# Kernel tuning notes

Measured on AMD Instinct MI355X. Metric: run time of the kernel, lower is better.

The kernel has to match this reference:

```python
import jax, jax.numpy as jnp
import numpy as np

N_NODES = 50000
N_EDGES = 600000
VOCAB = 32000
D = 128


def setup_inputs() -> dict:
    key = jax.random.key(0)
    ks = jax.random.split(key, 9)
    return {
        "emb_table": jax.random.normal(ks[0], (VOCAB, D), dtype=jnp.float32),
        "w1": jax.random.normal(ks[1], (D, D), dtype=jnp.float32) * (1.0 / np.sqrt(D)),
        "bias1": jax.random.normal(ks[2], (D,), dtype=jnp.float32),
        "w2": jax.random.normal(ks[3], (D, D), dtype=jnp.float32) * (1.0 / np.sqrt(D)),
        "bias2": jax.random.normal(ks[4], (D,), dtype=jnp.float32),
        "node_tokens": jax.random.randint(ks[5], (N_NODES,), 0, VOCAB, dtype=jnp.int32),
        "edge_tokens": jax.random.randint(ks[6], (N_EDGES,), 0, VOCAB, dtype=jnp.int32),
        "src": jax.random.randint(ks[7], (N_EDGES,), 0, N_NODES, dtype=jnp.int32),
        "dst": jax.random.randint(ks[8], (N_EDGES,), 0, N_NODES, dtype=jnp.int32),
    }


def reference(emb_table, w1, bias1, w2, bias2, node_tokens, edge_tokens, src, dst):
    # Embedding lookup + affine + relu for nodes and edges
    node_h = jax.nn.relu(emb_table[node_tokens] @ w1 + bias1)   # [N, D]
    edge_h = jax.nn.relu(emb_table[edge_tokens] @ w2 + bias2)   # [E, D]
    # DGL update_all(u_mul_e, sum): gather src node h, mul with edge h, scatter-sum to dst
    msg = node_h[src] * edge_h                                  # [E, D]
    out = jax.ops.segment_sum(msg, dst, num_segments=N_NODES)   # [N, D]
    return out
```

## Files before the change

### kernel.cpp

```cpp
#include <hip/hip_runtime.h>

#define VOCAB   32000
#define D       128
#define NNODES  50000
#define NEDGES  600000

typedef unsigned short ushort_t;
typedef unsigned int   uint_t;

__device__ __forceinline__ float bf2f(ushort_t u) {
    union { uint_t i; float f; } c; c.i = ((uint_t)u) << 16; return c.f;
}
__device__ __forceinline__ ushort_t f2bf(float f) {
    union { float f; uint_t i; } c; c.f = f;
    uint_t u = c.i;
    u += 0x7fff + ((u >> 16) & 1);
    return (ushort_t)(u >> 16);
}

__global__ __launch_bounds__(256) void mlp_hist_kernel(
    const float* __restrict__ emb,
    const float* __restrict__ w1, const float* __restrict__ b1,
    const float* __restrict__ w2, const float* __restrict__ b2,
    ushort_t* __restrict__ t1, ushort_t* __restrict__ t2,
    const int* __restrict__ dstv, int* __restrict__ counts)
{
    {
        const int base = blockIdx.x * (NEDGES / 1000);
        for (int i = base + threadIdx.x; i < base + NEDGES / 1000; i += 256)
            atomicAdd(&counts[dstv[i]], 1);
    }

    const int tab = (blockIdx.x >= 500) ? 1 : 0;
    const float* __restrict__ w = tab ? w2 : w1;
    const float* __restrict__ b = tab ? b2 : b1;
    ushort_t* __restrict__ outt = tab ? t2 : t1;
    const int bid = blockIdx.x - tab * 500;

    __shared__ __align__(16) float wT[D * D];

    {
        const int k0 = threadIdx.x >> 5;
        const int c4 = (threadIdx.x & 31) * 4;
        for (int kk = 0; kk < D; kk += 8) {
            const int k = kk + k0;
            const float4 v = *(const float4*)(w + (size_t)k * D + c4);
            const float vv[4] = {v.x, v.y, v.z, v.w};
            #pragma unroll
            for (int j = 0; j < 4; ++j) {
                const int c = c4 + j;
                const int g = (k >> 2) ^ (c & 7);
                wT[c * D + g * 4 + (k & 3)] = vv[j];
            }
        }
    }

    const int lane = threadIdx.x & 63;
    const int sub  = threadIdx.x >> 6;
    const int c0 = lane, c1 = lane + 64;
    const float bb0 = b[c0], bb1 = b[c1];
    const int s0 = (c0 & 7), s1 = (c1 & 7);
    __syncthreads();

    for (int it = 0; it < 4; ++it) {
        const int rowbase = __builtin_amdgcn_readfirstlane(
            (it * 500 + bid) * 16 + sub * 4);
        const float* __restrict__ x0 = emb + (size_t)rowbase * D;

        float acc[4][2];
        #pragma unroll
        for (int j = 0; j < 4; ++j) { acc[j][0] = bb0; acc[j][1] = bb1; }

        #pragma unroll 2
        for (int kc = 0; kc < 16; ++kc) {
            const int g0 = kc * 2, g1 = kc * 2 + 1;
            const float4 w0a = *(const float4*)&wT[c0 * D + ((g0 ^ s0) << 2)];
            const float4 w0b = *(const float4*)&wT[c0 * D + ((g1 ^ s0) << 2)];
            const float4 w1a = *(const float4*)&wT[c1 * D + ((g0 ^ s1) << 2)];
            const float4 w1b = *(const float4*)&wT[c1 * D + ((g1 ^ s1) << 2)];
            #pragma unroll
            for (int j = 0; j < 4; ++j) {
                const float* __restrict__ xr = x0 + j * D + kc * 8;
                const float4 xa = *(const float4*)(xr);
                const float4 xb = *(const float4*)(xr + 4);
                acc[j][0] = fmaf(xa.x, w0a.x, acc[j][0]);
                acc[j][1] = fmaf(xa.x, w1a.x, acc[j][1]);
                acc[j][0] = fmaf(xa.y, w0a.y, acc[j][0]);
                acc[j][1] = fmaf(xa.y, w1a.y, acc[j][1]);
                acc[j][0] = fmaf(xa.z, w0a.z, acc[j][0]);
                acc[j][1] = fmaf(xa.z, w1a.z, acc[j][1]);
                acc[j][0] = fmaf(xa.w, w0a.w, acc[j][0]);
                acc[j][1] = fmaf(xa.w, w1a.w, acc[j][1]);
                acc[j][0] = fmaf(xb.x, w0b.x, acc[j][0]);
                acc[j][1] = fmaf(xb.x, w1b.x, acc[j][1]);
                acc[j][0] = fmaf(xb.y, w0b.y, acc[j][0]);
                acc[j][1] = fmaf(xb.y, w1b.y, acc[j][1]);
                acc[j][0] = fmaf(xb.z, w0b.z, acc[j][0]);
                acc[j][1] = fmaf(xb.z, w1b.z, acc[j][1]);
                acc[j][0] = fmaf(xb.w, w0b.w, acc[j][0]);
                acc[j][1] = fmaf(xb.w, w1b.w, acc[j][1]);
            }
        }
        #pragma unroll
        for (int j = 0; j < 4; ++j) {
            ushort_t* o = outt + (size_t)(rowbase + j) * D;
            o[c0] = f2bf(fmaxf(acc[j][0], 0.f));
            o[c1] = f2bf(fmaxf(acc[j][1], 0.f));
        }
    }
}

__global__ __launch_bounds__(256) void scan_phase1(
    const int* __restrict__ counts,
    int* __restrict__ offs,
    int* __restrict__ btot)
{
    const int i    = blockIdx.x * 256 + threadIdx.x;
    const int lane = threadIdx.x & 63;
    const int wv   = threadIdx.x >> 6;

    const int v = (i < NNODES) ? counts[i] : 0;
    int inc = v;
    #pragma unroll
    for (int off = 1; off < 64; off <<= 1) {
        int u = __shfl_up(inc, off);
        if (lane >= off) inc += u;
    }
    __shared__ int wtot[4];
    if (lane == 63) wtot[wv] = inc;
    __syncthreads();
    int wpre = 0;
    #pragma unroll
    for (int k = 0; k < 3; ++k) if (k < wv) wpre += wtot[k];
    inc += wpre;
    if (i < NNODES) offs[i] = inc - v;
    if (threadIdx.x == 255) btot[blockIdx.x] = inc;
}

__global__ __launch_bounds__(256) void scan_phase2(
    const int* __restrict__ btot,
    int* __restrict__ offs,
    int* __restrict__ cursor,
    int nblocks)
{
    const int t    = threadIdx.x;
    const int lane = t & 63;
    const int wv   = t >> 6;

    int v = (t < blockIdx.x && t < nblocks) ? btot[t] : 0;
    #pragma unroll
    for (int off = 32; off > 0; off >>= 1) v += __shfl_xor(v, off);
    __shared__ int ws[4];
    if (lane == 0) ws[wv] = v;
    __syncthreads();
    const int bpre = ws[0] + ws[1] + ws[2] + ws[3];

    const int i = blockIdx.x * 256 + t;
    if (i < NNODES) {
        const int o = offs[i] + bpre;
        offs[i]   = o;
        cursor[i] = o;
    }
    if (blockIdx.x == 0 && t == 0) offs[NNODES] = NEDGES;
}

__global__ __launch_bounds__(256) void scatter_kernel(
    const int4* __restrict__ src4, const int4* __restrict__ dst4,
    const int* __restrict__ node_tokens, const int4* __restrict__ et4,
    int* __restrict__ cursor, uint_t* __restrict__ pairs)
{
    const int t = blockIdx.x * 256 + threadIdx.x;
    if (t >= NEDGES / 4) return;
    const int4 s = src4[t];
    const int4 d = dst4[t];
    const int4 te = et4[t];
    int p;
    p = atomicAdd(&cursor[d.x], 1);
    pairs[p] = (uint_t)node_tokens[s.x] | ((uint_t)te.x << 16);
    p = atomicAdd(&cursor[d.y], 1);
    pairs[p] = (uint_t)node_tokens[s.y] | ((uint_t)te.y << 16);
    p = atomicAdd(&cursor[d.z], 1);
    pairs[p] = (uint_t)node_tokens[s.z] | ((uint_t)te.z << 16);
    p = atomicAdd(&cursor[d.w], 1);
    pairs[p] = (uint_t)node_tokens[s.w] | ((uint_t)te.w << 16);
}

__global__ __launch_bounds__(256) void gather_kernel(
    const ushort_t* __restrict__ t1, const ushort_t* __restrict__ t2,
    const int* __restrict__ offsets, const uint_t* __restrict__ pairs,
    float* __restrict__ outp)
{
    const int wid = (blockIdx.x * 256 + threadIdx.x) >> 6;
    if (wid >= NNODES) return;
    const int lane = threadIdx.x & 63;
    const int half = lane >> 5;
    const int sl   = lane & 31;

    const int beg = offsets[wid];
    const int end = offsets[wid + 1];

    float4 acc = {0.f, 0.f, 0.f, 0.f};
    for (int base = beg; base < end; base += 64) {
        const int m = min(64, end - base);
        uint_t pr = (lane < m) ? pairs[base + lane] : 0u;
        for (int j = half; j < m; j += 2) {
            const uint_t v = (uint_t)__shfl((int)pr, j);
            const int tn = (int)(v & 0xffffu);
            const int te = (int)(v >> 16);
            const ushort4 a  = ((const ushort4*)(t1 + (size_t)tn * D))[sl];
            const ushort4 bb = ((const ushort4*)(t2 + (size_t)te * D))[sl];
            acc.x = fmaf(bf2f(a.x), bf2f(bb.x), acc.x);
            acc.y = fmaf(bf2f(a.y), bf2f(bb.y), acc.y);
            acc.z = fmaf(bf2f(a.z), bf2f(bb.z), acc.z);
            acc.w = fmaf(bf2f(a.w), bf2f(bb.w), acc.w);
        }
    }
    acc.x += __shfl_xor(acc.x, 32);
    acc.y += __shfl_xor(acc.y, 32);
    acc.z += __shfl_xor(acc.z, 32);
    acc.w += __shfl_xor(acc.w, 32);
    if (half == 0)
        ((float4*)(outp + (size_t)wid * D))[sl] = acc;
}

extern "C" void kernel_launch(void* const* d_in, const int* in_sizes, int n_in,
                              void* d_out, int out_size, void* d_ws, size_t ws_size,
                              hipStream_t stream) {
    const float* emb = (const float*)d_in[0];
    const float* w1  = (const float*)d_in[1];
    const float* b1  = (const float*)d_in[2];
    const float* w2  = (const float*)d_in[3];
    const float* b2  = (const float*)d_in[4];
    const int* node_tokens = (const int*)d_in[5];
    const int* edge_tokens = (const int*)d_in[6];
    const int* src = (const int*)d_in[7];
    const int* dst = (const int*)d_in[8];
    float* out = (float*)d_out;

    char* wsb = (char*)d_ws;
    ushort_t* t1     = (ushort_t*)(wsb);
    ushort_t* t2     = (ushort_t*)(wsb +  8192000);
    uint_t*   pairs  = (uint_t*)  (wsb + 16384000);
    int*      counts = (int*)     (wsb + 18784000);
    int*      offs   = (int*)     (wsb + 18984000);
    int*      cursor = (int*)     (wsb + 19184016);
    int*      btot   = (int*)     (wsb + 19384016);

    hipMemsetAsync(counts, 0, NNODES * sizeof(int), stream);

    mlp_hist_kernel<<<1000, 256, 0, stream>>>(emb, w1, b1, w2, b2,
                                              t1, t2, dst, counts);

    const int nscan = (NNODES + 255) / 256;
    scan_phase1<<<nscan, 256, 0, stream>>>(counts, offs, btot);
    scan_phase2<<<nscan, 256, 0, stream>>>(btot, offs, cursor, nscan);
    scatter_kernel<<<(NEDGES / 4 + 255) / 256, 256, 0, stream>>>(
        (const int4*)src, (const int4*)dst, node_tokens,
        (const int4*)edge_tokens, cursor, pairs);

    gather_kernel<<<(NNODES + 3) / 4, 256, 0, stream>>>(t1, t2, offs, pairs, out);
}
```

Baseline: 242.8 us.

## Compute vocab-table MLP with bf16 MFMA instead of scalar FMA

Replaces the scalar-FMA dense layer that precomputes relu(emb@W+b) for the whole vocab with bf16 MFMA 16x16x32 instructions. Weights are held in registers as B fragments and loaded directly from global memory, so the shared-memory transpose and the barrier go away. Each wave computes one 64-column half of one table (w1 or w2). The embeddings and weights are rounded to bf16 before the multiply, which adds rounding error compared with the fp32 FMA path.

```diff
diff --git a/kernel.cpp b/kernel.cpp
--- a/kernel.cpp
+++ b/kernel.cpp
@@ -7,6 +7,8 @@
 
 typedef unsigned short ushort_t;
 typedef unsigned int   uint_t;
+typedef __attribute__((ext_vector_type(8))) __bf16 bf16x8;
+typedef __attribute__((ext_vector_type(4))) float  f32x4;
 
 __device__ __forceinline__ float bf2f(ushort_t u) {
     union { uint_t i; float f; } c; c.i = ((uint_t)u) << 16; return c.f;
@@ -18,7 +20,9 @@
     return (ushort_t)(u >> 16);
 }
 
-__global__ __launch_bounds__(256) void mlp_hist_kernel(
+union PkAB { uint_t u[4]; bf16x8 v; };
+
+__global__ __launch_bounds__(256) void mlp_mfma_hist_kernel(
     const float* __restrict__ emb,
     const float* __restrict__ w1, const float* __restrict__ b1,
     const float* __restrict__ w2, const float* __restrict__ b2,
@@ -31,81 +35,74 @@
             atomicAdd(&counts[dstv[i]], 1);
     }
 
-    const int tab = (blockIdx.x >= 500) ? 1 : 0;
-    const float* __restrict__ w = tab ? w2 : w1;
-    const float* __restrict__ b = tab ? b2 : b1;
-    ushort_t* __restrict__ outt = tab ? t2 : t1;
-    const int bid = blockIdx.x - tab * 500;
-
-    __shared__ __align__(16) float wT[D * D];
-
-    {
-        const int k0 = threadIdx.x >> 5;
-        const int c4 = (threadIdx.x & 31) * 4;
-        for (int kk = 0; kk < D; kk += 8) {
-            const int k = kk + k0;
-            const float4 v = *(const float4*)(w + (size_t)k * D + c4);
-            const float vv[4] = {v.x, v.y, v.z, v.w};
+    const int wv   = threadIdx.x >> 6;
+    const int lane = threadIdx.x & 63;
+    const int jcol = lane & 15;
+    const int krow = (lane >> 4) * 8;
+
+    const float* __restrict__ wsel = (wv >= 2) ? w2 : w1;
+    const float* __restrict__ bsel = (wv >= 2) ? b2 : b1;
+    ushort_t*    __restrict__ osel = (wv >= 2) ? t2 : t1;
+    const int colT = (wv & 1) * 64;
+
+    PkAB bfrag[4][4];
+    #pragma unroll
+    for (int n = 0; n < 4; ++n) {
+        const int c = colT + n * 16 + jcol;
+        #pragma unroll
+        for (int kk = 0; kk < 4; ++kk) {
+            const int k0 = kk * 32 + krow;
+            #pragma unroll
+            for (int e = 0; e < 4; ++e) {
+                const float lo = wsel[(size_t)(k0 + 2 * e)     * D + c];
+                const float hi = wsel[(size_t)(k0 + 2 * e + 1) * D + c];
+                bfrag[n][kk].u[e] = (uint_t)f2bf(lo) | ((uint_t)f2bf(hi) << 16);
+            }
+        }
+    }
+
+    float bval[4];
+    #pragma unroll
+    for (int n = 0; n < 4; ++n) bval[n] = bsel[colT + n * 16 + jcol];
+
+    #pragma unroll
+    for (int it = 0; it < 2; ++it) {
+        const int rowbase = (it * 1000 + blockIdx.x) * 16;
+        const float* __restrict__ aptr =
+            emb + (size_t)(rowbase + jcol) * D + krow;
+
+        PkAB afrag[4];
+        #pragma unroll
+        for (int kk = 0; kk < 4; ++kk) {
+            const float4 xa = *(const float4*)(aptr + kk * 32);
+            const float4 xb = *(const float4*)(aptr + kk * 32 + 4);
+            afrag[kk].u[0] = (uint_t)f2bf(xa.x) | ((uint_t)f2bf(xa.y) << 16);
+            afrag[kk].u[1] = (uint_t)f2bf(xa.z) | ((uint_t)f2bf(xa.w) << 16);
+            afrag[kk].u[2] = (uint_t)f2bf(xb.x) | ((uint_t)f2bf(xb.y) << 16);
+            afrag[kk].u[3] = (uint_t)f2bf(xb.z) | ((uint_t)f2bf(xb.w) << 16);
+        }
+
+        f32x4 acc[4];
+        #pragma unroll
+        for (int n = 0; n < 4; ++n)
+            acc[n] = (f32x4){bval[n], bval[n], bval[n], bval[n]};
+
+        #pragma unroll
+        for (int kk = 0; kk < 4; ++kk) {
+            #pragma unroll
+            for (int n = 0; n < 4; ++n)
+                acc[n] = __builtin_amdgcn_mfma_f32_16x16x32_bf16(
+                    afrag[kk].v, bfrag[n][kk].v, acc[n], 0, 0, 0);
+        }
+
+        #pragma unroll
+        for (int n = 0; n < 4; ++n) {
             #pragma unroll
             for (int j = 0; j < 4; ++j) {
-                const int c = c4 + j;
-                const int g = (k >> 2) ^ (c & 7);
-                wT[c * D + g * 4 + (k & 3)] = vv[j];
+                const int row = rowbase + (lane >> 4) * 4 + j;
+                osel[(size_t)row * D + colT + n * 16 + jcol] =
+                    f2bf(fmaxf(acc[n][j], 0.f));
             }
-        }
-    }
-
-    const int lane = threadIdx.x & 63;
-    const int sub  = threadIdx.x >> 6;
-    const int c0 = lane, c1 = lane + 64;
-    const float bb0 = b[c0], bb1 = b[c1];
-    const int s0 = (c0 & 7), s1 = (c1 & 7);
-    __syncthreads();
-
-    for (int it = 0; it < 4; ++it) {
-        const int rowbase = __builtin_amdgcn_readfirstlane(
-            (it * 500 + bid) * 16 + sub * 4);
-        const float* __restrict__ x0 = emb + (size_t)rowbase * D;
-
-        float acc[4][2];
-        #pragma unroll
-        for (int j = 0; j < 4; ++j) { acc[j][0] = bb0; acc[j][1] = bb1; }
-
-        #pragma unroll 2
-        for (int kc = 0; kc < 16; ++kc) {
-            const int g0 = kc * 2, g1 = kc * 2 + 1;
-            const float4 w0a = *(const float4*)&wT[c0 * D + ((g0 ^ s0) << 2)];
-            const float4 w0b = *(const float4*)&wT[c0 * D + ((g1 ^ s0) << 2)];
-            const float4 w1a = *(const float4*)&wT[c1 * D + ((g0 ^ s1) << 2)];
-            const float4 w1b = *(const float4*)&wT[c1 * D + ((g1 ^ s1) << 2)];
-            #pragma unroll
-            for (int j = 0; j < 4; ++j) {
-                const float* __restrict__ xr = x0 + j * D + kc * 8;
-                const float4 xa = *(const float4*)(xr);
-                const float4 xb = *(const float4*)(xr + 4);
-                acc[j][0] = fmaf(xa.x, w0a.x, acc[j][0]);
-                acc[j][1] = fmaf(xa.x, w1a.x, acc[j][1]);
-                acc[j][0] = fmaf(xa.y, w0a.y, acc[j][0]);
-                acc[j][1] = fmaf(xa.y, w1a.y, acc[j][1]);
-                acc[j][0] = fmaf(xa.z, w0a.z, acc[j][0]);
-                acc[j][1] = fmaf(xa.z, w1a.z, acc[j][1]);
-                acc[j][0] = fmaf(xa.w, w0a.w, acc[j][0]);
-                acc[j][1] = fmaf(xa.w, w1a.w, acc[j][1]);
-                acc[j][0] = fmaf(xb.x, w0b.x, acc[j][0]);
-                acc[j][1] = fmaf(xb.x, w1b.x, acc[j][1]);
-                acc[j][0] = fmaf(xb.y, w0b.y, acc[j][0]);
-                acc[j][1] = fmaf(xb.y, w1b.y, acc[j][1]);
-                acc[j][0] = fmaf(xb.z, w0b.z, acc[j][0]);
-                acc[j][1] = fmaf(xb.z, w1b.z, acc[j][1]);
-                acc[j][0] = fmaf(xb.w, w0b.w, acc[j][0]);
-                acc[j][1] = fmaf(xb.w, w1b.w, acc[j][1]);
-            }
-        }
-        #pragma unroll
-        for (int j = 0; j < 4; ++j) {
-            ushort_t* o = outt + (size_t)(rowbase + j) * D;
-            o[c0] = f2bf(fmaxf(acc[j][0], 0.f));
-            o[c1] = f2bf(fmaxf(acc[j][1], 0.f));
         }
     }
 }
@@ -248,8 +245,8 @@
 
     hipMemsetAsync(counts, 0, NNODES * sizeof(int), stream);
 
-    mlp_hist_kernel<<<1000, 256, 0, stream>>>(emb, w1, b1, w2, b2,
-                                              t1, t2, dst, counts);
+    mlp_mfma_hist_kernel<<<1000, 256, 0, stream>>>(emb, w1, b1, w2, b2,
+                                                   t1, t2, dst, counts);
 
     const int nscan = (NNODES + 255) / 256;
     scan_phase1<<<nscan, 256, 0, stream>>>(counts, offs, btot);
```

New measurement: 207.7 us (median of 2 runs). -14.4%, faster.
